# Kernel optimization log

Measured on AMD Instinct MI355X. Metric: run time of the kernel, lower is better.

## Reference

```python
import jax, jax.numpy as jnp
import numpy as np

B, H, W, C = 16, 64, 64, 192
NUM_HEADS, KEY_DIM, KS = 8, 32, 3


def setup_inputs() -> dict:
    key = jax.random.key(0)
    ks = jax.random.split(key, 9)
    Ck = C + 2  # key/value input dim: patches concat 2 dist channels
    def w(k, shape, fan_in):
        return jax.random.normal(k, shape, jnp.float32) / np.float32(np.sqrt(fan_in))
    return {
        "x": jax.random.normal(ks[0], (B, H, W, C), jnp.float32),
        "Wq": w(ks[1], (C, NUM_HEADS, KEY_DIM), C),
        "bq": jnp.zeros((NUM_HEADS, KEY_DIM), jnp.float32),
        "Wk": w(ks[2], (Ck, NUM_HEADS, KEY_DIM), Ck),
        "bk": jnp.zeros((NUM_HEADS, KEY_DIM), jnp.float32),
        "Wv": w(ks[3], (Ck, NUM_HEADS, KEY_DIM), Ck),
        "bv": jnp.zeros((NUM_HEADS, KEY_DIM), jnp.float32),
        "Wo": w(ks[4], (NUM_HEADS, KEY_DIM, C), NUM_HEADS * KEY_DIM),
        "bo": jnp.zeros((C,), jnp.float32),
    }


def _local_window_kv(x, ks):
    # tf.image.extract_patches SAME (zero pad) -> [B,H,W,ks*ks,C]
    pad = ks // 2
    xp = jnp.pad(x, ((0, 0), (pad, pad), (pad, pad), (0, 0)))
    b, h, w, c = x.shape
    patches = jnp.stack(
        [xp[:, i:i + h, j:j + w, :] for i in range(ks) for j in range(ks)], axis=3
    )  # [B,H,W,ks*ks,C], row-major over window like extract_patches
    # relative distances: tf.meshgrid default 'xy', concat (dists[0], dists[1])
    r = jnp.arange(ks, dtype=x.dtype) - ks // 2
    dx, dy = jnp.meshgrid(r, r)  # 'xy' indexing, matches tf.meshgrid default
    dists = jnp.stack([dx, dy], axis=-1).reshape(ks * ks, 2)  # [9,2]
    dists = jnp.broadcast_to(dists, (b, h, w, ks * ks, 2))
    return jnp.concatenate([patches, dists], axis=-1)  # [B,H,W,9,C+2]


def reference(x, Wq, bq, Wk, bk, Wv, bv, Wo, bo):
    kv_in = _local_window_kv(x, KS)  # [B,H,W,9,C+2]
    # keras MultiHeadAttention projections
    q = jnp.einsum('bxyc,chd->bxyhd', x, Wq) + bq           # [B,H,W,h,d] (q_len=1)
    k = jnp.einsum('bxykc,chd->bxykhd', kv_in, Wk) + bk     # [B,H,W,9,h,d]
    v = jnp.einsum('bxykc,chd->bxykhd', kv_in, Wv) + bv
    scale = np.float32(1.0 / np.sqrt(KEY_DIM))
    scores = jnp.einsum('bxyhd,bxykhd->bxyhk', q, k) * scale  # [B,H,W,h,9]
    attn = jax.nn.softmax(scores, axis=-1)
    o = jnp.einsum('bxyhk,bxykhd->bxyhd', attn, v)
    return jnp.einsum('bxyhd,hdc->bxyc', o, Wo) + bo          # [B,H,W,C]
```

## Files before the change

### kernel.cpp

```cpp
#include <hip/hip_runtime.h>
#include <hip/hip_bf16.h>


typedef __bf16 bf16x8_t __attribute__((ext_vector_type(8)));
typedef float f32x4_t __attribute__((ext_vector_type(4)));

#define SCALE 0.17677669529663687f
#define QSTRIDE 864
#define ZROW 65536

static __device__ __forceinline__ unsigned short bfbits(float f) {
    return __builtin_bit_cast(unsigned short, __float2bfloat16(f));
}
static __device__ __forceinline__ float bf2f(unsigned short u) {
    return __bfloat162float(__builtin_bit_cast(__hip_bfloat16, u));
}
static __device__ __forceinline__ float lo16f(unsigned int u) {
    return __builtin_bit_cast(float, u << 16);
}
static __device__ __forceinline__ float hi16f(unsigned int u) {
    return __builtin_bit_cast(float, u & 0xffff0000u);
}

static __device__ __forceinline__ void gload_lds16(const void* g, void* l) {
    __builtin_amdgcn_global_load_lds((const __attribute__((address_space(1))) void*)g,
                                     (__attribute__((address_space(3))) void*)l, 16, 0, 0);
}

__global__ void k_convert_x(const float* __restrict__ x, ushort4* __restrict__ xb, int n4) {
    int i = blockIdx.x * blockDim.x + threadIdx.x;
    const int stride = gridDim.x * blockDim.x;
    const float4* x4 = reinterpret_cast<const float4*>(x);
    for (; i < n4; i += stride) {
        float4 v = x4[i];
        ushort4 o;
        o.x = bfbits(v.x); o.y = bfbits(v.y); o.z = bfbits(v.z); o.w = bfbits(v.w);
        xb[i] = o;
    }
}

__global__ void k_pack(const float* __restrict__ Wq, const float* __restrict__ Wk,
                       const float* __restrict__ Wv, const float* __restrict__ Wo,
                       const float* __restrict__ bq, const float* __restrict__ bk,
                       const float* __restrict__ bv,
                       __hip_bfloat16* __restrict__ WqkvT, __hip_bfloat16* __restrict__ WoT,
                       float* __restrict__ qkvBias, float* __restrict__ wvTab,
                       __hip_bfloat16* __restrict__ QKV) {
    const int idx = blockIdx.x * blockDim.x + threadIdx.x;
    const int T0 = 896 * 192;
    const int T1 = T0 + 192 * 256;
    const int T2 = T1 + 896;
    const int T3 = T2 + 768;
    const int T4 = T3 + QSTRIDE;
    if (idx < T0) {
        const int m = idx / 192, k = idx % 192;
        float v = 0.f;
        if (m < 256) {
            v = Wq[k * 256 + m] * SCALE;
        } else if (m < 768) {
            const int j = m - 256, g = j >> 3, r = j & 7;
            const int d = 4 * g + (r & 3);
            v = (r < 4) ? Wk[k * 256 + d] : Wv[k * 256 + d];
        } else if (m < 864) {
            const int j = m - 768, h = j / 12, n = j % 12;
            if (n < 9) {
                const float dj = (float)(n % 3 - 1), di = (float)(n / 3 - 1);
                float acc = 0.f;
                for (int d = 0; d < 32; ++d) {
                    const int c = h * 32 + d;
                    const float bkv = dj * Wk[192 * 256 + c] + di * Wk[193 * 256 + c] + bk[c];
                    acc += Wq[k * 256 + c] * bkv;
                }
                v = acc * SCALE;
            }
        }
        WqkvT[m * 192 + k] = __float2bfloat16(v);
    } else if (idx < T1) {
        const int j = idx - T0;
        const int c = j >> 8, hd = j & 255;
        WoT[j] = __float2bfloat16(Wo[hd * 192 + c]);
    } else if (idx < T2) {
        const int col = idx - T1;
        float v = 0.f;
        if (col < 256) v = bq[col] * SCALE;
        else if (col >= 768 && col < 864) {
            const int j = col - 768, h = j / 12, n = j % 12;
            if (n < 9) {
                const float dj = (float)(n % 3 - 1), di = (float)(n / 3 - 1);
                float acc = 0.f;
                for (int d = 0; d < 32; ++d) {
                    const int c = h * 32 + d;
                    const float bkv = dj * Wk[192 * 256 + c] + di * Wk[193 * 256 + c] + bk[c];
                    acc += bq[c] * bkv;
                }
                v = acc * SCALE;
            }
        }
        qkvBias[col] = v;
    } else if (idx < T3) {
        const int j = idx - T2;
        const int t = j >> 8, m = j & 255;
        float v;
        if (t == 0)      v = Wv[192 * 256 + m];
        else if (t == 1) v = Wv[193 * 256 + m];
        else             v = bv[m];
        wvTab[j] = v;
    } else if (idx < T4) {
        const int j = idx - T3;
        QKV[(size_t)ZROW * QSTRIDE + j] = __float2bfloat16(0.f);
    }
}

template<int BM, int BN, int WRN, int WCN, int KDIM, int NOUT, int NBX, bool OUTF32, bool BIAS>
__global__ __launch_bounds__(256) void k_gemm_lds(const __hip_bfloat16* __restrict__ A,
                          const __hip_bfloat16* __restrict__ BT,
                          void* __restrict__ Cout,
                          const float* __restrict__ bias, int ldc) {
    constexpr int WTR = BM / WRN;
    constexpr int WTC = BN / WCN;
    constexpr int FR = WTR / 16;
    constexpr int FC = WTC / 16;
    constexpr int NK = KDIM / 64;
    __shared__ __hip_bfloat16 sA[BM * 64];
    __shared__ __hip_bfloat16 sB[BN * 64];
    const int bid = blockIdx.x;
    const int s = (bid & 7) * ((int)gridDim.x >> 3) + (bid >> 3);
    const int by = s / NBX, bx = s - by * NBX;
    const int tid = threadIdx.x;
    const int wave = tid >> 6, lane = tid & 63;
    const int wr = wave / WCN, wc = wave % WCN;
    const long rowBase = (long)by * BM;
    const long colBase = (long)bx * BN;
    const int lr = lane & 15, lk = lane >> 4;
    const int rx = lr & 7;
    const int srow = lane >> 3;
    const int scolsw = ((lane & 7) ^ srow) * 8;

    f32x4_t acc[FR][FC] = {};
    for (int t = 0; t < NK; ++t) {
        const int k0 = t * 64;
        #pragma unroll
        for (int r = 0; r < BM / 32; ++r) {
            const int row0 = r * 32 + wave * 8;
            gload_lds16(A + (rowBase + row0 + srow) * KDIM + k0 + scolsw, sA + row0 * 64);
        }
        #pragma unroll
        for (int r = 0; r < BN / 32; ++r) {
            const int row0 = r * 32 + wave * 8;
            gload_lds16(BT + (colBase + row0 + srow) * KDIM + k0 + scolsw, sB + row0 * 64);
        }
        __syncthreads();
        #pragma unroll
        for (int kk = 0; kk < 2; ++kk) {
            const int pc = ((lk + kk * 4) ^ rx) * 8;
            bf16x8_t a[FR], b[FC];
            #pragma unroll
            for (int fr = 0; fr < FR; ++fr)
                a[fr] = *reinterpret_cast<const bf16x8_t*>(sA + (wr * WTR + fr * 16 + lr) * 64 + pc);
            #pragma unroll
            for (int fc = 0; fc < FC; ++fc)
                b[fc] = *reinterpret_cast<const bf16x8_t*>(sB + (wc * WTC + fc * 16 + lr) * 64 + pc);
            #pragma unroll
            for (int fr = 0; fr < FR; ++fr) {
                #pragma unroll
                for (int fc = 0; fc < FC; ++fc)
                    acc[fr][fc] = __builtin_amdgcn_mfma_f32_16x16x32_bf16(a[fr], b[fc], acc[fr][fc], 0, 0, 0);
            }
        }
        __syncthreads();
    }
    const int rowSub = (lane >> 4) * 4;
    const int colSub = lane & 15;
    #pragma unroll
    for (int fr = 0; fr < FR; ++fr) {
        #pragma unroll
        for (int fc = 0; fc < FC; ++fc) {
            const long col = colBase + wc * WTC + fc * 16 + colSub;
            if (col >= NOUT) continue;
            float bvv = BIAS ? bias[col] : 0.f;
            #pragma unroll
            for (int r = 0; r < 4; ++r) {
                const long row = rowBase + wr * WTR + fr * 16 + rowSub + r;
                float v = acc[fr][fc][r] + bvv;
                if constexpr (OUTF32) ((float*)Cout)[row * ldc + col] = v;
                else ((__hip_bfloat16*)Cout)[row * ldc + col] = __float2bfloat16(v);
            }
        }
    }
}

__global__ __launch_bounds__(256) void k_attn(const __hip_bfloat16* __restrict__ QKV,
                       const float* __restrict__ wvTab,
                       __hip_bfloat16* __restrict__ O) {
    const int wave = threadIdx.x >> 6;
    const int lane = threadIdx.x & 63;
    const int bid = blockIdx.x;
    const int sblk = (bid & 7) * 2048 + (bid >> 3);
    const int p = sblk * 4 + wave;
    const int y = (p >> 6) & 63;
    const int xq = p & 63;
    const int h = lane >> 3, dg = lane & 7;
    const int idx = h * 32 + dg * 4;
    const __hip_bfloat16* rowQ = QKV + (size_t)p * QSTRIDE;

    const ushort4 qu = *reinterpret_cast<const ushort4*>(rowQ + idx);
    const float q0 = bf2f(qu.x), q1 = bf2f(qu.y), q2 = bf2f(qu.z), q3 = bf2f(qu.w);

    const ushort4 qba = *reinterpret_cast<const ushort4*>(rowQ + 768 + 12 * h);
    const ushort4 qbb = *reinterpret_cast<const ushort4*>(rowQ + 772 + 12 * h);
    const unsigned short qbc = *reinterpret_cast<const unsigned short*>(rowQ + 776 + 12 * h);
    float qb[9] = { bf2f(qba.x), bf2f(qba.y), bf2f(qba.z), bf2f(qba.w),
                    bf2f(qbb.x), bf2f(qbb.y), bf2f(qbb.z), bf2f(qbb.w), bf2f(qbc) };

    const char* baseQ = reinterpret_cast<const char*>(QKV);
    const long rowByte = (long)p * (QSTRIDE * 2);
    const int laneOff = 512 + 128 * h + 16 * dg;
    uint4 kv[9];
    #pragma unroll
    for (int n = 0; n < 9; ++n) {
        const int di = n / 3 - 1, dj = n % 3 - 1;
        const int ny = y + di, nx = xq + dj;
        const bool inb = ((unsigned)ny < 64u) & ((unsigned)nx < 64u);
        const long off = inb ? rowByte + (long)((di * 64 + dj) * (QSTRIDE * 2))
                             : (long)ZROW * (QSTRIDE * 2);
        kv[n] = *reinterpret_cast<const uint4*>(baseQ + off + laneOff);
    }

    float sc[9];
    #pragma unroll
    for (int n = 0; n < 9; ++n) {
        const float k0 = lo16f(kv[n].x), k1 = hi16f(kv[n].x);
        const float k2 = lo16f(kv[n].y), k3 = hi16f(kv[n].y);
        float ss = fmaf(q0, k0, fmaf(q1, k1, fmaf(q2, k2, q3 * k3)));
        ss += __shfl_xor(ss, 1);
        ss += __shfl_xor(ss, 2);
        ss += __shfl_xor(ss, 4);
        sc[n] = ss + qb[n];
    }
    float mx = sc[0];
    #pragma unroll
    for (int n = 1; n < 9; ++n) mx = fmaxf(mx, sc[n]);
    float sum = 0.f;
    #pragma unroll
    for (int n = 0; n < 9; ++n) { sc[n] = __expf(sc[n] - mx); sum += sc[n]; }
    const float inv = 1.0f / sum;
    const float Ej = (sc[2] + sc[5] + sc[8]) - (sc[0] + sc[3] + sc[6]);
    const float Ei = (sc[6] + sc[7] + sc[8]) - (sc[0] + sc[1] + sc[2]);

    float o0 = 0.f, o1 = 0.f, o2 = 0.f, o3 = 0.f;
    #pragma unroll
    for (int n = 0; n < 9; ++n) {
        o0 = fmaf(sc[n], lo16f(kv[n].z), o0);
        o1 = fmaf(sc[n], hi16f(kv[n].z), o1);
        o2 = fmaf(sc[n], lo16f(kv[n].w), o2);
        o3 = fmaf(sc[n], hi16f(kv[n].w), o3);
    }
    const float4 w0 = *reinterpret_cast<const float4*>(wvTab + idx);
    const float4 w1 = *reinterpret_cast<const float4*>(wvTab + 256 + idx);
    const float4 w2 = *reinterpret_cast<const float4*>(wvTab + 512 + idx);
    o0 = fmaf(Ej, w0.x, fmaf(Ei, w1.x, o0)) * inv + w2.x;
    o1 = fmaf(Ej, w0.y, fmaf(Ei, w1.y, o1)) * inv + w2.y;
    o2 = fmaf(Ej, w0.z, fmaf(Ei, w1.z, o2)) * inv + w2.z;
    o3 = fmaf(Ej, w0.w, fmaf(Ei, w1.w, o3)) * inv + w2.w;

    ushort4 ov;
    ov.x = bfbits(o0); ov.y = bfbits(o1); ov.z = bfbits(o2); ov.w = bfbits(o3);
    *reinterpret_cast<ushort4*>(O + (size_t)p * 256 + idx) = ov;
}

extern "C" void kernel_launch(void* const* d_in, const int* in_sizes, int n_in,
                              void* d_out, int out_size, void* d_ws, size_t ws_size,
                              hipStream_t stream) {
    (void)in_sizes; (void)n_in; (void)out_size; (void)ws_size;
    const float* x  = (const float*)d_in[0];
    const float* Wq = (const float*)d_in[1];
    const float* bq = (const float*)d_in[2];
    const float* Wk = (const float*)d_in[3];
    const float* bk = (const float*)d_in[4];
    const float* Wv = (const float*)d_in[5];
    const float* bv = (const float*)d_in[6];
    const float* Wo = (const float*)d_in[7];
    const float* bo = (const float*)d_in[8];

    char* ws = (char*)d_ws;
    __hip_bfloat16* xb    = (__hip_bfloat16*)(ws + 0);
    __hip_bfloat16* O     = (__hip_bfloat16*)(ws + 0);
    __hip_bfloat16* QKV   = (__hip_bfloat16*)(ws + 33554432);
    __hip_bfloat16* WqkvT = (__hip_bfloat16*)(ws + 146802368);
    __hip_bfloat16* WoT   = (__hip_bfloat16*)(ws + 147146432);
    float* qkvBias        = (float*)(ws + 147244736);
    float* wvTab          = (float*)(ws + 147248320);

    k_convert_x<<<4096, 256, 0, stream>>>(x, (ushort4*)xb, 12582912 / 4);
    k_pack<<<874, 256, 0, stream>>>(Wq, Wk, Wv, Wo, bq, bk, bv, WqkvT, WoT, qkvBias, wvTab, QKV);
    k_gemm_lds<128, 128, 2, 2, 192, 864, 7, false, true>
        <<<3584, 256, 0, stream>>>(xb, WqkvT, (void*)QKV, qkvBias, QSTRIDE);
    k_attn<<<16384, 256, 0, stream>>>(QKV, wvTab, O);
    k_gemm_lds<128, 64, 2, 2, 256, 192, 3, true, true>
        <<<1536, 256, 0, stream>>>(O, WoT, d_out, bo, 192);
}
```

Before: 114.8 us.

## Process 2x2 pixel quads per wave to reuse neighbor K/V loads

The attention kernel now has each wave handle a 2x2 block of output pixels. It loads the shared 4x4 neighborhood of K/V rows once and reuses them for all four pixels' 3x3 windows, instead of loading 9 rows per pixel. The grid shrinks by four to match. This is meant to cut redundant global/L2 traffic, at the cost of more registers per thread (16 uint4 held live) and less parallelism.

```diff
diff --git a/kernel.cpp b/kernel.cpp
--- a/kernel.cpp
+++ b/kernel.cpp
@@ -195,77 +195,83 @@
     const int wave = threadIdx.x >> 6;
     const int lane = threadIdx.x & 63;
     const int bid = blockIdx.x;
-    const int sblk = (bid & 7) * 2048 + (bid >> 3);
-    const int p = sblk * 4 + wave;
-    const int y = (p >> 6) & 63;
-    const int xq = p & 63;
+    const int sblk = (bid & 7) * 512 + (bid >> 3);
+    const int qd = sblk * 4 + wave;
+    const int b = qd >> 10;
+    const int qy = (qd >> 5) & 31, qx = qd & 31;
+    const int y = qy << 1, x = qx << 1;
+    const int p00 = (b << 12) | (y << 6) | x;
     const int h = lane >> 3, dg = lane & 7;
     const int idx = h * 32 + dg * 4;
-    const __hip_bfloat16* rowQ = QKV + (size_t)p * QSTRIDE;
-
-    const ushort4 qu = *reinterpret_cast<const ushort4*>(rowQ + idx);
-    const float q0 = bf2f(qu.x), q1 = bf2f(qu.y), q2 = bf2f(qu.z), q3 = bf2f(qu.w);
-
-    const ushort4 qba = *reinterpret_cast<const ushort4*>(rowQ + 768 + 12 * h);
-    const ushort4 qbb = *reinterpret_cast<const ushort4*>(rowQ + 772 + 12 * h);
-    const unsigned short qbc = *reinterpret_cast<const unsigned short*>(rowQ + 776 + 12 * h);
-    float qb[9] = { bf2f(qba.x), bf2f(qba.y), bf2f(qba.z), bf2f(qba.w),
-                    bf2f(qbb.x), bf2f(qbb.y), bf2f(qbb.z), bf2f(qbb.w), bf2f(qbc) };
-
     const char* baseQ = reinterpret_cast<const char*>(QKV);
-    const long rowByte = (long)p * (QSTRIDE * 2);
     const int laneOff = 512 + 128 * h + 16 * dg;
-    uint4 kv[9];
+
+    uint4 kv[16];
     #pragma unroll
-    for (int n = 0; n < 9; ++n) {
-        const int di = n / 3 - 1, dj = n % 3 - 1;
-        const int ny = y + di, nx = xq + dj;
+    for (int m = 0; m < 16; ++m) {
+        const int rr = m >> 2, cc = m & 3;
+        const int ny = y + rr - 1, nx = x + cc - 1;
         const bool inb = ((unsigned)ny < 64u) & ((unsigned)nx < 64u);
-        const long off = inb ? rowByte + (long)((di * 64 + dj) * (QSTRIDE * 2))
-                             : (long)ZROW * (QSTRIDE * 2);
-        kv[n] = *reinterpret_cast<const uint4*>(baseQ + off + laneOff);
-    }
-
-    float sc[9];
-    #pragma unroll
-    for (int n = 0; n < 9; ++n) {
-        const float k0 = lo16f(kv[n].x), k1 = hi16f(kv[n].x);
-        const float k2 = lo16f(kv[n].y), k3 = hi16f(kv[n].y);
-        float ss = fmaf(q0, k0, fmaf(q1, k1, fmaf(q2, k2, q3 * k3)));
-        ss += __shfl_xor(ss, 1);
-        ss += __shfl_xor(ss, 2);
-        ss += __shfl_xor(ss, 4);
-        sc[n] = ss + qb[n];
-    }
-    float mx = sc[0];
-    #pragma unroll
-    for (int n = 1; n < 9; ++n) mx = fmaxf(mx, sc[n]);
-    float sum = 0.f;
-    #pragma unroll
-    for (int n = 0; n < 9; ++n) { sc[n] = __expf(sc[n] - mx); sum += sc[n]; }
-    const float inv = 1.0f / sum;
-    const float Ej = (sc[2] + sc[5] + sc[8]) - (sc[0] + sc[3] + sc[6]);
-    const float Ei = (sc[6] + sc[7] + sc[8]) - (sc[0] + sc[1] + sc[2]);
-
-    float o0 = 0.f, o1 = 0.f, o2 = 0.f, o3 = 0.f;
-    #pragma unroll
-    for (int n = 0; n < 9; ++n) {
-        o0 = fmaf(sc[n], lo16f(kv[n].z), o0);
-        o1 = fmaf(sc[n], hi16f(kv[n].z), o1);
-        o2 = fmaf(sc[n], lo16f(kv[n].w), o2);
-        o3 = fmaf(sc[n], hi16f(kv[n].w), o3);
-    }
+        const long row = inb ? (long)((b << 12) | (ny << 6) | nx) : (long)ZROW;
+        kv[m] = *reinterpret_cast<const uint4*>(baseQ + row * (QSTRIDE * 2) + laneOff);
+    }
+
     const float4 w0 = *reinterpret_cast<const float4*>(wvTab + idx);
     const float4 w1 = *reinterpret_cast<const float4*>(wvTab + 256 + idx);
     const float4 w2 = *reinterpret_cast<const float4*>(wvTab + 512 + idx);
-    o0 = fmaf(Ej, w0.x, fmaf(Ei, w1.x, o0)) * inv + w2.x;
-    o1 = fmaf(Ej, w0.y, fmaf(Ei, w1.y, o1)) * inv + w2.y;
-    o2 = fmaf(Ej, w0.z, fmaf(Ei, w1.z, o2)) * inv + w2.z;
-    o3 = fmaf(Ej, w0.w, fmaf(Ei, w1.w, o3)) * inv + w2.w;
-
-    ushort4 ov;
-    ov.x = bfbits(o0); ov.y = bfbits(o1); ov.z = bfbits(o2); ov.w = bfbits(o3);
-    *reinterpret_cast<ushort4*>(O + (size_t)p * 256 + idx) = ov;
+
+    #pragma unroll
+    for (int pxi = 0; pxi < 4; ++pxi) {
+        const int dy = pxi >> 1, dx = pxi & 1;
+        const int p = p00 + dy * 64 + dx;
+        const __hip_bfloat16* rowQ = QKV + (size_t)p * QSTRIDE;
+        const ushort4 qu = *reinterpret_cast<const ushort4*>(rowQ + idx);
+        const ushort4 qa = *reinterpret_cast<const ushort4*>(rowQ + 768 + 12 * h);
+        const ushort4 qbv = *reinterpret_cast<const ushort4*>(rowQ + 772 + 12 * h);
+        const unsigned short qc = *reinterpret_cast<const unsigned short*>(rowQ + 776 + 12 * h);
+        const float q0 = bf2f(qu.x), q1 = bf2f(qu.y), q2 = bf2f(qu.z), q3 = bf2f(qu.w);
+        const float qb[9] = { bf2f(qa.x), bf2f(qa.y), bf2f(qa.z), bf2f(qa.w),
+                              bf2f(qbv.x), bf2f(qbv.y), bf2f(qbv.z), bf2f(qbv.w), bf2f(qc) };
+
+        float sc[9];
+        #pragma unroll
+        for (int n = 0; n < 9; ++n) {
+            const int m = (dy + n / 3) * 4 + dx + n % 3;
+            const uint4 k = kv[m];
+            float s = fmaf(q0, lo16f(k.x), fmaf(q1, hi16f(k.x),
+                      fmaf(q2, lo16f(k.y), q3 * hi16f(k.y))));
+            s += __shfl_xor(s, 1);
+            s += __shfl_xor(s, 2);
+            s += __shfl_xor(s, 4);
+            sc[n] = s + qb[n];
+        }
+        float mx = sc[0];
+        #pragma unroll
+        for (int n = 1; n < 9; ++n) mx = fmaxf(mx, sc[n]);
+        float sum = 0.f;
+        #pragma unroll
+        for (int n = 0; n < 9; ++n) { sc[n] = __expf(sc[n] - mx); sum += sc[n]; }
+        const float inv = 1.0f / sum;
+        const float Ej = (sc[2] + sc[5] + sc[8]) - (sc[0] + sc[3] + sc[6]);
+        const float Ei = (sc[6] + sc[7] + sc[8]) - (sc[0] + sc[1] + sc[2]);
+
+        float o0 = 0.f, o1 = 0.f, o2 = 0.f, o3 = 0.f;
+        #pragma unroll
+        for (int n = 0; n < 9; ++n) {
+            const int m = (dy + n / 3) * 4 + dx + n % 3;
+            const uint4 k = kv[m];
+            o0 = fmaf(sc[n], lo16f(k.z), o0);
+            o1 = fmaf(sc[n], hi16f(k.z), o1);
+            o2 = fmaf(sc[n], lo16f(k.w), o2);
+            o3 = fmaf(sc[n], hi16f(k.w), o3);
+        }
+        ushort4 ov;
+        ov.x = bfbits(fmaf(Ej, w0.x, fmaf(Ei, w1.x, o0)) * inv + w2.x);
+        ov.y = bfbits(fmaf(Ej, w0.y, fmaf(Ei, w1.y, o1)) * inv + w2.y);
+        ov.z = bfbits(fmaf(Ej, w0.z, fmaf(Ei, w1.z, o2)) * inv + w2.z);
+        ov.w = bfbits(fmaf(Ej, w0.w, fmaf(Ei, w1.w, o3)) * inv + w2.w);
+        *reinterpret_cast<ushort4*>(O + (size_t)p * 256 + idx) = ov;
+    }
 }
 
 extern "C" void kernel_launch(void* const* d_in, const int* in_sizes, int n_in,
@@ -295,7 +301,7 @@
     k_pack<<<874, 256, 0, stream>>>(Wq, Wk, Wv, Wo, bq, bk, bv, WqkvT, WoT, qkvBias, wvTab, QKV);
     k_gemm_lds<128, 128, 2, 2, 192, 864, 7, false, true>
         <<<3584, 256, 0, stream>>>(xb, WqkvT, (void*)QKV, qkvBias, QSTRIDE);
-    k_attn<<<16384, 256, 0, stream>>>(QKV, wvTab, O);
+    k_attn<<<4096, 256, 0, stream>>>(QKV, wvTab, O);
     k_gemm_lds<128, 64, 2, 2, 256, 192, 3, true, true>
         <<<1536, 256, 0, stream>>>(O, WoT, d_out, bo, 192);
 }
```

Measured after the change: 113.7 us. Within noise of the previous version (-0.9%).
